# Kernel optimization log

Hardware: AMD Instinct MI355X
Metric: run time of the kernel (lower is better)

Reference implementation:

```python
import jax, jax.numpy as jnp
import numpy as np

DIM = 512
HEADS = 8
HEAD_DIM = DIM // HEADS

def setup_inputs() -> dict:
    key = jax.random.key(0)
    ks = jax.random.split(key, 5)
    s = 1.0 / np.sqrt(DIM)
    x = jax.random.normal(ks[0], (4, 2048, DIM), dtype=jnp.float32)
    w_qkv = jax.random.uniform(ks[1], (DIM, 3 * DIM), jnp.float32, -s, s)
    b_qkv = jax.random.uniform(ks[2], (3 * DIM,), jnp.float32, -s, s)
    w_out = jax.random.uniform(ks[3], (DIM, DIM), jnp.float32, -s, s)
    b_out = jax.random.uniform(ks[4], (DIM,), jnp.float32, -s, s)
    return {"x": x, "w_qkv": w_qkv, "b_qkv": b_qkv, "w_out": w_out, "b_out": b_out}

def reference(x, w_qkv, b_qkv, w_out, b_out):
    B, N, D = x.shape
    qkv = x @ w_qkv + b_qkv  # [B, N, 3D]
    qkv = qkv.reshape(B, N, 3, HEADS, HEAD_DIM).transpose(2, 0, 3, 1, 4)  # [3, B, H, N, hd]
    q, k, v = qkv[0], qkv[1], qkv[2]
    scale = 1.0 / np.sqrt(HEAD_DIM).astype(np.float32)
    attn = jnp.einsum('bhqd,bhkd->bhqk', q, k) * scale
    attn = jax.nn.softmax(attn, axis=-1)
    out = jnp.einsum('bhqk,bhkd->bhqd', attn, v)  # [B, H, N, hd]
    out = out.transpose(0, 2, 1, 3).reshape(B, N, D)
    return out @ w_out + b_out
```

## Files before the change

kernel.cpp:

```cpp
#include <hip/hip_runtime.h>

#define NB 4
#define NH 8
#define HD 64
#define DIMV 512
#define NSEQ 2048
#define QKVLD 1536
#define NTOK (NB*NSEQ)
#define KVB 64
#define QSCALE 0.18033688011112042f

typedef __attribute__((ext_vector_type(8))) short s8v;
typedef __attribute__((ext_vector_type(4))) float f4v;

typedef __attribute__((address_space(1))) void gvoid;
typedef __attribute__((address_space(3))) void lvoid;

__device__ __forceinline__ void load_lds16(const void* g, void* l){
  __builtin_amdgcn_global_load_lds((gvoid*)(void*)g, (lvoid*)l, 16, 0, 0);
}

__device__ __forceinline__ ushort f2bf(float f){
  unsigned u = __float_as_uint(f);
  u += 0x7fffu + ((u >> 16) & 1u);
  return (ushort)(u >> 16);
}

__device__ __forceinline__ unsigned pk2bf(float a, float b){
  return (unsigned)f2bf(a) | ((unsigned)f2bf(b) << 16);
}

__device__ __forceinline__ unsigned cvt_pk_bf16(float lo, float hi){
  unsigned r;
  asm("v_cvt_pk_bf16_f32 %0, %1, %2" : "=v"(r) : "v"(lo), "v"(hi));
  return r;
}
__device__ __forceinline__ float fexp2(float x){
  float r;
  asm("v_exp_f32 %0, %1" : "=v"(r) : "v"(x));
  return r;
}
__device__ __forceinline__ void plane32(unsigned &a, unsigned &b){
  asm("v_permlane32_swap_b32 %0, %1" : "+v"(a), "+v"(b));
}
__device__ __forceinline__ void plane16(unsigned &a, unsigned &b){
  asm("v_permlane16_swap_b32 %0, %1" : "+v"(a), "+v"(b));
}

__global__ __launch_bounds__(256) void k_prep(const float* __restrict__ x,
                                              ushort* __restrict__ xb,
                                              const float* __restrict__ w_qkv,
                                              ushort* __restrict__ wqkvT,
                                              const float* __restrict__ w_out,
                                              ushort* __restrict__ woutT){
  const int blk = blockIdx.x;
  const int tid = threadIdx.x;
  if (blk < 4096){
    const int i = blk * 256 + tid;
    float4 v = ((const float4*)x)[i];
    ushort4 o;
    o.x = f2bf(v.x); o.y = f2bf(v.y); o.z = f2bf(v.z); o.w = f2bf(v.w);
    ((ushort4*)xb)[i] = o;
    return;
  }
  __shared__ float t[32][33];
  const float* in; ushort* out; int C, bx, by;
  if (blk < 4864){
    const int idx = blk - 4096;
    in = w_qkv; out = wqkvT; C = QKVLD;
    bx = (idx % 48) * 32; by = (idx / 48) * 32;
  } else {
    const int idx = blk - 4864;
    in = w_out; out = woutT; C = DIMV;
    bx = (idx & 15) * 32; by = (idx >> 4) * 32;
  }
  const int tx = tid & 31, ty = tid >> 5;
  #pragma unroll
  for (int j = 0; j < 32; j += 8)
    t[ty + j][tx] = in[(size_t)(by + ty + j)*C + bx + tx];
  __syncthreads();
  #pragma unroll
  for (int j = 0; j < 32; j += 8)
    out[(size_t)(bx + ty + j)*DIMV + by + tx] = f2bf(t[tx][ty + j]);
}

template<int MODE, int NCT>
__global__ __launch_bounds__(256) void k_gemm(const ushort* __restrict__ A,
                                              const ushort* __restrict__ Bt,
                                              const float* __restrict__ bias,
                                              void* __restrict__ Cout,
                                              ushort* __restrict__ vtp,
                                              int N, int K){
  __shared__ ushort As[128*32];
  __shared__ ushort Bs[128*32];
  const int tid = threadIdx.x;
  const int w = tid >> 6, l = tid & 63;
  const int lr = l & 15, lg = l >> 4;
  const int wm = w >> 1, wn = w & 1;
  const int wg = blockIdx.x;
  const int xcd = wg & 7, idx = wg >> 3;
  const int tn = (idx % NCT) * 128;
  const int tm = (xcd * 8 + idx / NCT) * 128;
  const int srow = l >> 2;
  const int scol = (l & 3) * 8;
  f4v acc[4][4] = {};

  for (int kk = 0; kk < K; kk += 32){
    __syncthreads();
    #pragma unroll
    for (int c = 0; c < 2; ++c){
      const int r = (w*2 + c)*16 + srow;
      load_lds16(A  + (size_t)(tm + r)*K + kk + scol, (char*)As + (w*2 + c)*1024);
      load_lds16(Bt + (size_t)(tn + r)*K + kk + scol, (char*)Bs + (w*2 + c)*1024);
    }
    __syncthreads();
    s8v af[4], bf[4];
    #pragma unroll
    for (int i = 0; i < 4; ++i){
      af[i] = *(const s8v*)(&As[(wm*64 + i*16 + lr)*32 + lg*8]);
      bf[i] = *(const s8v*)(&Bs[(wn*64 + i*16 + lr)*32 + lg*8]);
    }
    #pragma unroll
    for (int mi = 0; mi < 4; ++mi)
      #pragma unroll
      for (int ni = 0; ni < 4; ++ni)
        acc[mi][ni] = __builtin_amdgcn_mfma_f32_16x16x32_bf16(af[mi], bf[ni], acc[mi][ni], 0, 0, 0);
  }

  if (MODE == 0){
    ushort* C = (ushort*)Cout;
    if (tn >= 2*DIMV){
      const int b = tm >> 11;
      const int n0 = (tm & (NSEQ-1)) + wm*64;
      #pragma unroll
      for (int ni = 0; ni < 4; ++ni){
        const int c = tn + wn*64 + ni*16 + lr;
        const int hd_i = c - 2*DIMV;
        const float bv = bias[c];
        ushort* vrow = vtp + ((size_t)(b*DIMV + hd_i))*NSEQ;
        #pragma unroll
        for (int mi = 0; mi < 4; ++mi){
          const int n = n0 + mi*16 + lg*4;
          uint2 pk;
          pk.x = pk2bf(acc[mi][ni][0] + bv, acc[mi][ni][1] + bv);
          pk.y = pk2bf(acc[mi][ni][2] + bv, acc[mi][ni][3] + bv);
          *(uint2*)(vrow + n) = pk;
        }
      }
    } else {
      #pragma unroll
      for (int ni = 0; ni < 4; ++ni){
        const int c = tn + wn*64 + ni*16 + lr;
        const float bv = bias[c];
        const float sc = (c < DIMV) ? QSCALE : 1.0f;
        #pragma unroll
        for (int mi = 0; mi < 4; ++mi)
          #pragma unroll
          for (int i = 0; i < 4; ++i){
            const int r = tm + wm*64 + mi*16 + lg*4 + i;
            C[(size_t)r*N + c] = f2bf((acc[mi][ni][i] + bv) * sc);
          }
      }
    }
  } else {
    float* C = (float*)Cout;
    #pragma unroll
    for (int ni = 0; ni < 4; ++ni){
      const int c = tn + wn*64 + ni*16 + lr;
      const float bv = bias[c];
      #pragma unroll
      for (int mi = 0; mi < 4; ++mi)
        #pragma unroll
        for (int i = 0; i < 4; ++i){
          const int r = tm + wm*64 + mi*16 + lg*4 + i;
          C[(size_t)r*N + c] = acc[mi][ni][i] + bv;
        }
    }
  }
}

__global__ __launch_bounds__(256, 4) void k_attn(const ushort* __restrict__ qkv,
                                                 const ushort* __restrict__ vt,
                                                 ushort* __restrict__ ao){
  __shared__ alignas(1024) char smem[2][16384];
  const int tid = threadIdx.x;
  const int w = tid >> 6, l = tid & 63;
  const int lr = l & 15, lg = l >> 4;
  const int wg = blockIdx.x;
  const int n = (wg & 7) * 128 + (wg >> 3);
  const int bh = n >> 5, xt = n & 31;
  const int b = bh >> 3, h = bh & 7;
  const int q0 = xt * 64 + w * 16;

  const ushort* qp = qkv + (size_t)(b*NSEQ + q0 + lr)*QKVLD + h*HD + lg*8;
  const s8v qf0 = *(const s8v*)(qp);
  const s8v qf1 = *(const s8v*)(qp + 32);

  const int r8 = l >> 3;
  const int lc = (l & 7) ^ r8;
  const int wbase = w * 16;
  const ushort* kg0 = qkv + (size_t)(b*NSEQ + wbase + r8)*QKVLD + DIMV + h*HD + lc*8;
  const ushort* kg1 = kg0 + (size_t)8*QKVLD;
  const ushort* vg0 = vt + (size_t)(bh*HD + wbase + r8)*NSEQ + lc*8;
  const ushort* vg1 = vg0 + (size_t)8*NSEQ;

  float lsum = 0.0f;
  f4v o[4] = {};

  load_lds16(kg0, &smem[0][ wbase   *128]);
  load_lds16(kg1, &smem[0][(wbase+8)*128]);
  load_lds16(vg0, &smem[0][ wbase   *128 + 8192]);
  load_lds16(vg1, &smem[0][(wbase+8)*128 + 8192]);
  kg0 += (size_t)KVB*QKVLD; kg1 += (size_t)KVB*QKVLD; vg0 += KVB; vg1 += KVB;

  const int swz = (lr & 7) << 4;
  const int ro0 = lr*128 + ((     lg*16) ^ swz);
  const int ro1 = lr*128 + ((64 + lg*16) ^ swz);

  #pragma unroll 2
  for (int kt = 0; kt < NSEQ/KVB; ++kt){
    const int cur = kt & 1;
    __syncthreads();

    if (kt + 1 < NSEQ/KVB){
      char* dst = &smem[cur^1][0];
      load_lds16(kg0, dst +  wbase   *128);
      load_lds16(kg1, dst + (wbase+8)*128);
      load_lds16(vg0, dst +  wbase   *128 + 8192);
      load_lds16(vg1, dst + (wbase+8)*128 + 8192);
      kg0 += (size_t)KVB*QKVLD; kg1 += (size_t)KVB*QKVLD; vg0 += KVB; vg1 += KVB;
    }

    const char* b0 = &smem[cur][0] + ro0;
    const char* b1 = &smem[cur][0] + ro1;

    f4v s0 = {0.f,0.f,0.f,0.f}, s1 = {0.f,0.f,0.f,0.f};
    f4v s2 = {0.f,0.f,0.f,0.f}, s3 = {0.f,0.f,0.f,0.f};
    __builtin_amdgcn_s_setprio(1);
    {
      const s8v a0 = *(const s8v*)(b0 +    0), a1 = *(const s8v*)(b1 +    0);
      const s8v a2 = *(const s8v*)(b0 + 2048), a3 = *(const s8v*)(b1 + 2048);
      s0 = __builtin_amdgcn_mfma_f32_16x16x32_bf16(a0, qf0, s0, 0,0,0);
      s0 = __builtin_amdgcn_mfma_f32_16x16x32_bf16(a1, qf1, s0, 0,0,0);
      s1 = __builtin_amdgcn_mfma_f32_16x16x32_bf16(a2, qf0, s1, 0,0,0);
      s1 = __builtin_amdgcn_mfma_f32_16x16x32_bf16(a3, qf1, s1, 0,0,0);
    }
    {
      const s8v a0 = *(const s8v*)(b0 + 4096), a1 = *(const s8v*)(b1 + 4096);
      const s8v a2 = *(const s8v*)(b0 + 6144), a3 = *(const s8v*)(b1 + 6144);
      s2 = __builtin_amdgcn_mfma_f32_16x16x32_bf16(a0, qf0, s2, 0,0,0);
      s2 = __builtin_amdgcn_mfma_f32_16x16x32_bf16(a1, qf1, s2, 0,0,0);
      s3 = __builtin_amdgcn_mfma_f32_16x16x32_bf16(a2, qf0, s3, 0,0,0);
      s3 = __builtin_amdgcn_mfma_f32_16x16x32_bf16(a3, qf1, s3, 0,0,0);
    }
    __builtin_amdgcn_s_setprio(0);

    union { uint4 u; s8v v; } pf0, pf1;
    {
      const float p0 = fexp2(s0[0]), p1 = fexp2(s0[1]);
      const float p2 = fexp2(s0[2]), p3 = fexp2(s0[3]);
      const float p4 = fexp2(s1[0]), p5 = fexp2(s1[1]);
      const float p6 = fexp2(s1[2]), p7 = fexp2(s1[3]);
      lsum += ((p0 + p1) + (p2 + p3)) + ((p4 + p5) + (p6 + p7));
      unsigned a = cvt_pk_bf16(p0, p1), bq = cvt_pk_bf16(p4, p5);
      plane32(a, bq); plane16(a, bq);
      unsigned c = cvt_pk_bf16(p2, p3), d = cvt_pk_bf16(p6, p7);
      plane32(c, d);  plane16(c, d);
      pf0.u.x = a; pf0.u.y = c; pf0.u.z = bq; pf0.u.w = d;
    }

    __builtin_amdgcn_s_setprio(1);
    {
      const s8v v0 = *(const s8v*)(b0 + 8192);
      const s8v v1 = *(const s8v*)(b0 + 10240);
      const s8v v2 = *(const s8v*)(b0 + 12288);
      const s8v v3 = *(const s8v*)(b0 + 14336);
      o[0] = __builtin_amdgcn_mfma_f32_16x16x32_bf16(v0, pf0.v, o[0], 0,0,0);
      o[1] = __builtin_amdgcn_mfma_f32_16x16x32_bf16(v1, pf0.v, o[1], 0,0,0);
      o[2] = __builtin_amdgcn_mfma_f32_16x16x32_bf16(v2, pf0.v, o[2], 0,0,0);
      o[3] = __builtin_amdgcn_mfma_f32_16x16x32_bf16(v3, pf0.v, o[3], 0,0,0);
    }
    __builtin_amdgcn_s_setprio(0);

    {
      const float p0 = fexp2(s2[0]), p1 = fexp2(s2[1]);
      const float p2 = fexp2(s2[2]), p3 = fexp2(s2[3]);
      const float p4 = fexp2(s3[0]), p5 = fexp2(s3[1]);
      const float p6 = fexp2(s3[2]), p7 = fexp2(s3[3]);
      lsum += ((p0 + p1) + (p2 + p3)) + ((p4 + p5) + (p6 + p7));
      unsigned a = cvt_pk_bf16(p0, p1), bq = cvt_pk_bf16(p4, p5);
      plane32(a, bq); plane16(a, bq);
      unsigned c = cvt_pk_bf16(p2, p3), d = cvt_pk_bf16(p6, p7);
      plane32(c, d);  plane16(c, d);
      pf1.u.x = a; pf1.u.y = c; pf1.u.z = bq; pf1.u.w = d;
    }

    __builtin_amdgcn_s_setprio(1);
    {
      const s8v v0 = *(const s8v*)(b1 + 8192);
      const s8v v1 = *(const s8v*)(b1 + 10240);
      const s8v v2 = *(const s8v*)(b1 + 12288);
      const s8v v3 = *(const s8v*)(b1 + 14336);
      o[0] = __builtin_amdgcn_mfma_f32_16x16x32_bf16(v0, pf1.v, o[0], 0,0,0);
      o[1] = __builtin_amdgcn_mfma_f32_16x16x32_bf16(v1, pf1.v, o[1], 0,0,0);
      o[2] = __builtin_amdgcn_mfma_f32_16x16x32_bf16(v2, pf1.v, o[2], 0,0,0);
      o[3] = __builtin_amdgcn_mfma_f32_16x16x32_bf16(v3, pf1.v, o[3], 0,0,0);
    }
    __builtin_amdgcn_s_setprio(0);
  }

  float lt = lsum;
  lt += __shfl_xor(lt, 16, 64);
  lt += __shfl_xor(lt, 32, 64);
  const float inv = 1.0f / lt;
  ushort* op = ao + (size_t)(b*NSEQ + q0 + lr)*DIMV + h*HD;
  #pragma unroll
  for (int ni = 0; ni < 4; ++ni){
    uint2 pk;
    pk.x = cvt_pk_bf16(o[ni][0]*inv, o[ni][1]*inv);
    pk.y = cvt_pk_bf16(o[ni][2]*inv, o[ni][3]*inv);
    *(uint2*)(op + ni*16 + lg*4) = pk;
  }
}


extern "C" void kernel_launch(void* const* d_in, const int* in_sizes, int n_in,
                              void* d_out, int out_size, void* d_ws, size_t ws_size,
                              hipStream_t stream) {
  (void)in_sizes; (void)n_in; (void)out_size; (void)ws_size;
  const float* x     = (const float*)d_in[0];
  const float* w_qkv = (const float*)d_in[1];
  const float* b_qkv = (const float*)d_in[2];
  const float* w_out = (const float*)d_in[3];
  const float* b_out = (const float*)d_in[4];
  float* out = (float*)d_out;

  char* ws = (char*)d_ws;
  ushort* xb    = (ushort*)(ws);
  ushort* wqkvT = (ushort*)(ws + 8388608);
  ushort* woutT = (ushort*)(ws + 8388608 + 1572864);
  ushort* qkv   = (ushort*)(ws + 10485760);
  ushort* vt    = (ushort*)(ws + 35651584);
  ushort* ao    = (ushort*)(ws + 44040192);

  k_prep<<<dim3(4096 + 768 + 256), 256, 0, stream>>>(x, xb, w_qkv, wqkvT, w_out, woutT);
  k_gemm<0,12><<<dim3(768), 256, 0, stream>>>(xb, wqkvT, b_qkv, qkv, vt, QKVLD, DIMV);
  k_attn<<<dim3(32*NB*NH), 256, 0, stream>>>(qkv, vt, ao);
  k_gemm<1,4><<<dim3(256), 256, 0, stream>>>(ao, woutT, b_out, out, nullptr, DIMV, DIMV);
}
```

Baseline: 103.3 us.

## Load V tiles directly from global into registers instead of staging in LDS

The attention kernel now fetches the transposed V fragments straight from global memory into registers each iteration, and shared memory is halved to hold only K tiles. This removes LDS staging and LDS reads for V and may raise occupancy, since each of the four waves reads the same V. In exchange, every wave issues redundant global loads for V, and their latency sits inside the loop with no prefetch ahead of the PV MMAs. The PV MMAs are also reordered to run together after both softmax blocks.

```diff
diff --git a/kernel.cpp b/kernel.cpp
--- a/kernel.cpp
+++ b/kernel.cpp
@@ -182,7 +182,7 @@
 __global__ __launch_bounds__(256, 4) void k_attn(const ushort* __restrict__ qkv,
                                                  const ushort* __restrict__ vt,
                                                  ushort* __restrict__ ao){
-  __shared__ alignas(1024) char smem[2][16384];
+  __shared__ alignas(1024) char smem[2][8192];
   const int tid = threadIdx.x;
   const int w = tid >> 6, l = tid & 63;
   const int lr = l & 15, lg = l >> 4;
@@ -201,17 +201,18 @@
   const int wbase = w * 16;
   const ushort* kg0 = qkv + (size_t)(b*NSEQ + wbase + r8)*QKVLD + DIMV + h*HD + lc*8;
   const ushort* kg1 = kg0 + (size_t)8*QKVLD;
-  const ushort* vg0 = vt + (size_t)(bh*HD + wbase + r8)*NSEQ + lc*8;
-  const ushort* vg1 = vg0 + (size_t)8*NSEQ;
+
+  const ushort* vp0 = vt + (size_t)(bh*HD +  0 + lr)*NSEQ + lg*8;
+  const ushort* vp1 = vt + (size_t)(bh*HD + 16 + lr)*NSEQ + lg*8;
+  const ushort* vp2 = vt + (size_t)(bh*HD + 32 + lr)*NSEQ + lg*8;
+  const ushort* vp3 = vt + (size_t)(bh*HD + 48 + lr)*NSEQ + lg*8;
 
   float lsum = 0.0f;
   f4v o[4] = {};
 
   load_lds16(kg0, &smem[0][ wbase   *128]);
   load_lds16(kg1, &smem[0][(wbase+8)*128]);
-  load_lds16(vg0, &smem[0][ wbase   *128 + 8192]);
-  load_lds16(vg1, &smem[0][(wbase+8)*128 + 8192]);
-  kg0 += (size_t)KVB*QKVLD; kg1 += (size_t)KVB*QKVLD; vg0 += KVB; vg1 += KVB;
+  kg0 += (size_t)KVB*QKVLD; kg1 += (size_t)KVB*QKVLD;
 
   const int swz = (lr & 7) << 4;
   const int ro0 = lr*128 + ((     lg*16) ^ swz);
@@ -222,13 +223,17 @@
     const int cur = kt & 1;
     __syncthreads();
 
+    const s8v vv00 = *(const s8v*)(vp0), vv01 = *(const s8v*)(vp0 + 32);
+    const s8v vv10 = *(const s8v*)(vp1), vv11 = *(const s8v*)(vp1 + 32);
+    const s8v vv20 = *(const s8v*)(vp2), vv21 = *(const s8v*)(vp2 + 32);
+    const s8v vv30 = *(const s8v*)(vp3), vv31 = *(const s8v*)(vp3 + 32);
+    vp0 += KVB; vp1 += KVB; vp2 += KVB; vp3 += KVB;
+
     if (kt + 1 < NSEQ/KVB){
       char* dst = &smem[cur^1][0];
       load_lds16(kg0, dst +  wbase   *128);
       load_lds16(kg1, dst + (wbase+8)*128);
-      load_lds16(vg0, dst +  wbase   *128 + 8192);
-      load_lds16(vg1, dst + (wbase+8)*128 + 8192);
-      kg0 += (size_t)KVB*QKVLD; kg1 += (size_t)KVB*QKVLD; vg0 += KVB; vg1 += KVB;
+      kg0 += (size_t)KVB*QKVLD; kg1 += (size_t)KVB*QKVLD;
     }
 
     const char* b0 = &smem[cur][0] + ro0;
@@ -268,20 +273,6 @@
       plane32(c, d);  plane16(c, d);
       pf0.u.x = a; pf0.u.y = c; pf0.u.z = bq; pf0.u.w = d;
     }
-
-    __builtin_amdgcn_s_setprio(1);
-    {
-      const s8v v0 = *(const s8v*)(b0 + 8192);
-      const s8v v1 = *(const s8v*)(b0 + 10240);
-      const s8v v2 = *(const s8v*)(b0 + 12288);
-      const s8v v3 = *(const s8v*)(b0 + 14336);
-      o[0] = __builtin_amdgcn_mfma_f32_16x16x32_bf16(v0, pf0.v, o[0], 0,0,0);
-      o[1] = __builtin_amdgcn_mfma_f32_16x16x32_bf16(v1, pf0.v, o[1], 0,0,0);
-      o[2] = __builtin_amdgcn_mfma_f32_16x16x32_bf16(v2, pf0.v, o[2], 0,0,0);
-      o[3] = __builtin_amdgcn_mfma_f32_16x16x32_bf16(v3, pf0.v, o[3], 0,0,0);
-    }
-    __builtin_amdgcn_s_setprio(0);
-
     {
       const float p0 = fexp2(s2[0]), p1 = fexp2(s2[1]);
       const float p2 = fexp2(s2[2]), p3 = fexp2(s2[3]);
@@ -296,16 +287,14 @@
     }
 
     __builtin_amdgcn_s_setprio(1);
-    {
-      const s8v v0 = *(const s8v*)(b1 + 8192);
-      const s8v v1 = *(const s8v*)(b1 + 10240);
-      const s8v v2 = *(const s8v*)(b1 + 12288);
-      const s8v v3 = *(const s8v*)(b1 + 14336);
-      o[0] = __builtin_amdgcn_mfma_f32_16x16x32_bf16(v0, pf1.v, o[0], 0,0,0);
-      o[1] = __builtin_amdgcn_mfma_f32_16x16x32_bf16(v1, pf1.v, o[1], 0,0,0);
-      o[2] = __builtin_amdgcn_mfma_f32_16x16x32_bf16(v2, pf1.v, o[2], 0,0,0);
-      o[3] = __builtin_amdgcn_mfma_f32_16x16x32_bf16(v3, pf1.v, o[3], 0,0,0);
-    }
+    o[0] = __builtin_amdgcn_mfma_f32_16x16x32_bf16(vv00, pf0.v, o[0], 0,0,0);
+    o[1] = __builtin_amdgcn_mfma_f32_16x16x32_bf16(vv10, pf0.v, o[1], 0,0,0);
+    o[2] = __builtin_amdgcn_mfma_f32_16x16x32_bf16(vv20, pf0.v, o[2], 0,0,0);
+    o[3] = __builtin_amdgcn_mfma_f32_16x16x32_bf16(vv30, pf0.v, o[3], 0,0,0);
+    o[0] = __builtin_amdgcn_mfma_f32_16x16x32_bf16(vv01, pf1.v, o[0], 0,0,0);
+    o[1] = __builtin_amdgcn_mfma_f32_16x16x32_bf16(vv11, pf1.v, o[1], 0,0,0);
+    o[2] = __builtin_amdgcn_mfma_f32_16x16x32_bf16(vv21, pf1.v, o[2], 0,0,0);
+    o[3] = __builtin_amdgcn_mfma_f32_16x16x32_bf16(vv31, pf1.v, o[3], 0,0,0);
     __builtin_amdgcn_s_setprio(0);
   }
 
```

Result: slower. 183.7 us (+77.9%).

## Process two 16-row query tiles per wave in attention to reuse K/V fragments

Applied to the files above, without the earlier changes.

Each wave in the attention kernel now handles 32 query rows (two 16-row MFMA tiles) instead of 16. Each block therefore covers 128 queries, and the grid halves to 512 blocks. Every K and V fragment read from LDS is reused by two MFMAs, which halves LDS traffic and K/V global loads per query. The cost is more registers (launch bounds lowered to 2 blocks per CU) and fewer blocks, which cuts occupancy and parallelism on a 256-CU device.

```diff
diff --git a/kernel.cpp b/kernel.cpp
--- a/kernel.cpp
+++ b/kernel.cpp
@@ -179,7 +179,7 @@
   }
 }
 
-__global__ __launch_bounds__(256, 4) void k_attn(const ushort* __restrict__ qkv,
+__global__ __launch_bounds__(256, 2) void k_attn(const ushort* __restrict__ qkv,
                                                  const ushort* __restrict__ vt,
                                                  ushort* __restrict__ ao){
   __shared__ alignas(1024) char smem[2][16384];
@@ -187,14 +187,17 @@
   const int w = tid >> 6, l = tid & 63;
   const int lr = l & 15, lg = l >> 4;
   const int wg = blockIdx.x;
-  const int n = (wg & 7) * 128 + (wg >> 3);
-  const int bh = n >> 5, xt = n & 31;
+  const int n = (wg & 7) * 64 + (wg >> 3);
+  const int bh = n >> 4, xt = n & 15;
   const int b = bh >> 3, h = bh & 7;
-  const int q0 = xt * 64 + w * 16;
-
-  const ushort* qp = qkv + (size_t)(b*NSEQ + q0 + lr)*QKVLD + h*HD + lg*8;
-  const s8v qf0 = *(const s8v*)(qp);
-  const s8v qf1 = *(const s8v*)(qp + 32);
+  const int q0 = xt * 128 + w * 32;
+
+  const ushort* qpA = qkv + (size_t)(b*NSEQ + q0 + lr)*QKVLD + h*HD + lg*8;
+  const ushort* qpB = qpA + (size_t)16*QKVLD;
+  const s8v qfA0 = *(const s8v*)(qpA);
+  const s8v qfA1 = *(const s8v*)(qpA + 32);
+  const s8v qfB0 = *(const s8v*)(qpB);
+  const s8v qfB1 = *(const s8v*)(qpB + 32);
 
   const int r8 = l >> 3;
   const int lc = (l & 7) ^ r8;
@@ -204,8 +207,8 @@
   const ushort* vg0 = vt + (size_t)(bh*HD + wbase + r8)*NSEQ + lc*8;
   const ushort* vg1 = vg0 + (size_t)8*NSEQ;
 
-  float lsum = 0.0f;
-  f4v o[4] = {};
+  float lsumA = 0.0f, lsumB = 0.0f;
+  f4v oA[4] = {}, oB[4] = {};
 
   load_lds16(kg0, &smem[0][ wbase   *128]);
   load_lds16(kg1, &smem[0][(wbase+8)*128]);
@@ -217,7 +220,6 @@
   const int ro0 = lr*128 + ((     lg*16) ^ swz);
   const int ro1 = lr*128 + ((64 + lg*16) ^ swz);
 
-  #pragma unroll 2
   for (int kt = 0; kt < NSEQ/KVB; ++kt){
     const int cur = kt & 1;
     __syncthreads();
@@ -234,92 +236,101 @@
     const char* b0 = &smem[cur][0] + ro0;
     const char* b1 = &smem[cur][0] + ro1;
 
-    f4v s0 = {0.f,0.f,0.f,0.f}, s1 = {0.f,0.f,0.f,0.f};
-    f4v s2 = {0.f,0.f,0.f,0.f}, s3 = {0.f,0.f,0.f,0.f};
+    f4v sA[4] = {}, sB[4] = {};
     __builtin_amdgcn_s_setprio(1);
+    #pragma unroll
+    for (int kb = 0; kb < 4; ++kb){
+      const s8v kf0 = *(const s8v*)(b0 + kb*2048);
+      const s8v kf1 = *(const s8v*)(b1 + kb*2048);
+      sA[kb] = __builtin_amdgcn_mfma_f32_16x16x32_bf16(kf0, qfA0, sA[kb], 0,0,0);
+      sA[kb] = __builtin_amdgcn_mfma_f32_16x16x32_bf16(kf1, qfA1, sA[kb], 0,0,0);
+      sB[kb] = __builtin_amdgcn_mfma_f32_16x16x32_bf16(kf0, qfB0, sB[kb], 0,0,0);
+      sB[kb] = __builtin_amdgcn_mfma_f32_16x16x32_bf16(kf1, qfB1, sB[kb], 0,0,0);
+    }
+    __builtin_amdgcn_s_setprio(0);
+
+    union { uint4 u; s8v v; } pfA0, pfA1, pfB0, pfB1;
     {
-      const s8v a0 = *(const s8v*)(b0 +    0), a1 = *(const s8v*)(b1 +    0);
-      const s8v a2 = *(const s8v*)(b0 + 2048), a3 = *(const s8v*)(b1 + 2048);
-      s0 = __builtin_amdgcn_mfma_f32_16x16x32_bf16(a0, qf0, s0, 0,0,0);
-      s0 = __builtin_amdgcn_mfma_f32_16x16x32_bf16(a1, qf1, s0, 0,0,0);
-      s1 = __builtin_amdgcn_mfma_f32_16x16x32_bf16(a2, qf0, s1, 0,0,0);
-      s1 = __builtin_amdgcn_mfma_f32_16x16x32_bf16(a3, qf1, s1, 0,0,0);
-    }
-    {
-      const s8v a0 = *(const s8v*)(b0 + 4096), a1 = *(const s8v*)(b1 + 4096);
-      const s8v a2 = *(const s8v*)(b0 + 6144), a3 = *(const s8v*)(b1 + 6144);
-      s2 = __builtin_amdgcn_mfma_f32_16x16x32_bf16(a0, qf0, s2, 0,0,0);
-      s2 = __builtin_amdgcn_mfma_f32_16x16x32_bf16(a1, qf1, s2, 0,0,0);
-      s3 = __builtin_amdgcn_mfma_f32_16x16x32_bf16(a2, qf0, s3, 0,0,0);
-      s3 = __builtin_amdgcn_mfma_f32_16x16x32_bf16(a3, qf1, s3, 0,0,0);
-    }
-    __builtin_amdgcn_s_setprio(0);
-
-    union { uint4 u; s8v v; } pf0, pf1;
-    {
-      const float p0 = fexp2(s0[0]), p1 = fexp2(s0[1]);
-      const float p2 = fexp2(s0[2]), p3 = fexp2(s0[3]);
-      const float p4 = fexp2(s1[0]), p5 = fexp2(s1[1]);
-      const float p6 = fexp2(s1[2]), p7 = fexp2(s1[3]);
-      lsum += ((p0 + p1) + (p2 + p3)) + ((p4 + p5) + (p6 + p7));
+      const float p0 = fexp2(sA[0][0]), p1 = fexp2(sA[0][1]);
+      const float p2 = fexp2(sA[0][2]), p3 = fexp2(sA[0][3]);
+      const float p4 = fexp2(sA[1][0]), p5 = fexp2(sA[1][1]);
+      const float p6 = fexp2(sA[1][2]), p7 = fexp2(sA[1][3]);
+      lsumA += ((p0 + p1) + (p2 + p3)) + ((p4 + p5) + (p6 + p7));
       unsigned a = cvt_pk_bf16(p0, p1), bq = cvt_pk_bf16(p4, p5);
       plane32(a, bq); plane16(a, bq);
       unsigned c = cvt_pk_bf16(p2, p3), d = cvt_pk_bf16(p6, p7);
       plane32(c, d);  plane16(c, d);
-      pf0.u.x = a; pf0.u.y = c; pf0.u.z = bq; pf0.u.w = d;
-    }
-
-    __builtin_amdgcn_s_setprio(1);
+      pfA0.u.x = a; pfA0.u.y = c; pfA0.u.z = bq; pfA0.u.w = d;
+    }
     {
-      const s8v v0 = *(const s8v*)(b0 + 8192);
-      const s8v v1 = *(const s8v*)(b0 + 10240);
-      const s8v v2 = *(const s8v*)(b0 + 12288);
-      const s8v v3 = *(const s8v*)(b0 + 14336);
-      o[0] = __builtin_amdgcn_mfma_f32_16x16x32_bf16(v0, pf0.v, o[0], 0,0,0);
-      o[1] = __builtin_amdgcn_mfma_f32_16x16x32_bf16(v1, pf0.v, o[1], 0,0,0);
-      o[2] = __builtin_amdgcn_mfma_f32_16x16x32_bf16(v2, pf0.v, o[2], 0,0,0);
-      o[3] = __builtin_amdgcn_mfma_f32_16x16x32_bf16(v3, pf0.v, o[3], 0,0,0);
-    }
-    __builtin_amdgcn_s_setprio(0);
-
-    {
-      const float p0 = fexp2(s2[0]), p1 = fexp2(s2[1]);
-      const float p2 = fexp2(s2[2]), p3 = fexp2(s2[3]);
-      const float p4 = fexp2(s3[0]), p5 = fexp2(s3[1]);
-      const float p6 = fexp2(s3[2]), p7 = fexp2(s3[3]);
-      lsum += ((p0 + p1) + (p2 + p3)) + ((p4 + p5) + (p6 + p7));
+      const float p0 = fexp2(sA[2][0]), p1 = fexp2(sA[2][1]);
+      const float p2 = fexp2(sA[2][2]), p3 = fexp2(sA[2][3]);
+      const float p4 = fexp2(sA[3][0]), p5 = fexp2(sA[3][1]);
+      const float p6 = fexp2(sA[3][2]), p7 = fexp2(sA[3][3]);
+      lsumA += ((p0 + p1) + (p2 + p3)) + ((p4 + p5) + (p6 + p7));
       unsigned a = cvt_pk_bf16(p0, p1), bq = cvt_pk_bf16(p4, p5);
       plane32(a, bq); plane16(a, bq);
       unsigned c = cvt_pk_bf16(p2, p3), d = cvt_pk_bf16(p6, p7);
       plane32(c, d);  plane16(c, d);
-      pf1.u.x = a; pf1.u.y = c; pf1.u.z = bq; pf1.u.w = d;
+      pfA1.u.x = a; pfA1.u.y = c; pfA1.u.z = bq; pfA1.u.w = d;
+    }
+    {
+      const float p0 = fexp2(sB[0][0]), p1 = fexp2(sB[0][1]);
+      const float p2 = fexp2(sB[0][2]), p3 = fexp2(sB[0][3]);
+      const float p4 = fexp2(sB[1][0]), p5 = fexp2(sB[1][1]);
+      const float p6 = fexp2(sB[1][2]), p7 = fexp2(sB[1][3]);
+      lsumB += ((p0 + p1) + (p2 + p3)) + ((p4 + p5) + (p6 + p7));
+      unsigned a = cvt_pk_bf16(p0, p1), bq = cvt_pk_bf16(p4, p5);
+      plane32(a, bq); plane16(a, bq);
+      unsigned c = cvt_pk_bf16(p2, p3), d = cvt_pk_bf16(p6, p7);
+      plane32(c, d);  plane16(c, d);
+      pfB0.u.x = a; pfB0.u.y = c; pfB0.u.z = bq; pfB0.u.w = d;
+    }
+    {
+      const float p0 = fexp2(sB[2][0]), p1 = fexp2(sB[2][1]);
+      const float p2 = fexp2(sB[2][2]), p3 = fexp2(sB[2][3]);
+      const float p4 = fexp2(sB[3][0]), p5 = fexp2(sB[3][1]);
+      const float p6 = fexp2(sB[3][2]), p7 = fexp2(sB[3][3]);
+      lsumB += ((p0 + p1) + (p2 + p3)) + ((p4 + p5) + (p6 + p7));
+      unsigned a = cvt_pk_bf16(p0, p1), bq = cvt_pk_bf16(p4, p5);
+      plane32(a, bq); plane16(a, bq);
+      unsigned c = cvt_pk_bf16(p2, p3), d = cvt_pk_bf16(p6, p7);
+      plane32(c, d);  plane16(c, d);
+      pfB1.u.x = a; pfB1.u.y = c; pfB1.u.z = bq; pfB1.u.w = d;
     }
 
     __builtin_amdgcn_s_setprio(1);
-    {
-      const s8v v0 = *(const s8v*)(b1 + 8192);
-      const s8v v1 = *(const s8v*)(b1 + 10240);
-      const s8v v2 = *(const s8v*)(b1 + 12288);
-      const s8v v3 = *(const s8v*)(b1 + 14336);
-      o[0] = __builtin_amdgcn_mfma_f32_16x16x32_bf16(v0, pf1.v, o[0], 0,0,0);
-      o[1] = __builtin_amdgcn_mfma_f32_16x16x32_bf16(v1, pf1.v, o[1], 0,0,0);
-      o[2] = __builtin_amdgcn_mfma_f32_16x16x32_bf16(v2, pf1.v, o[2], 0,0,0);
-      o[3] = __builtin_amdgcn_mfma_f32_16x16x32_bf16(v3, pf1.v, o[3], 0,0,0);
+    #pragma unroll
+    for (int ni = 0; ni < 4; ++ni){
+      const s8v vf0 = *(const s8v*)(b0 + 8192 + ni*2048);
+      const s8v vf1 = *(const s8v*)(b1 + 8192 + ni*2048);
+      oA[ni] = __builtin_amdgcn_mfma_f32_16x16x32_bf16(vf0, pfA0.v, oA[ni], 0,0,0);
+      oA[ni] = __builtin_amdgcn_mfma_f32_16x16x32_bf16(vf1, pfA1.v, oA[ni], 0,0,0);
+      oB[ni] = __builtin_amdgcn_mfma_f32_16x16x32_bf16(vf0, pfB0.v, oB[ni], 0,0,0);
+      oB[ni] = __builtin_amdgcn_mfma_f32_16x16x32_bf16(vf1, pfB1.v, oB[ni], 0,0,0);
     }
     __builtin_amdgcn_s_setprio(0);
   }
 
-  float lt = lsum;
-  lt += __shfl_xor(lt, 16, 64);
-  lt += __shfl_xor(lt, 32, 64);
-  const float inv = 1.0f / lt;
-  ushort* op = ao + (size_t)(b*NSEQ + q0 + lr)*DIMV + h*HD;
+  float ltA = lsumA;
+  ltA += __shfl_xor(ltA, 16, 64);
+  ltA += __shfl_xor(ltA, 32, 64);
+  float ltB = lsumB;
+  ltB += __shfl_xor(ltB, 16, 64);
+  ltB += __shfl_xor(ltB, 32, 64);
+  const float invA = 1.0f / ltA;
+  const float invB = 1.0f / ltB;
+  ushort* opA = ao + (size_t)(b*NSEQ + q0 + lr)*DIMV + h*HD;
+  ushort* opB = opA + (size_t)16*DIMV;
   #pragma unroll
   for (int ni = 0; ni < 4; ++ni){
     uint2 pk;
-    pk.x = cvt_pk_bf16(o[ni][0]*inv, o[ni][1]*inv);
-    pk.y = cvt_pk_bf16(o[ni][2]*inv, o[ni][3]*inv);
-    *(uint2*)(op + ni*16 + lg*4) = pk;
+    pk.x = cvt_pk_bf16(oA[ni][0]*invA, oA[ni][1]*invA);
+    pk.y = cvt_pk_bf16(oA[ni][2]*invA, oA[ni][3]*invA);
+    *(uint2*)(opA + ni*16 + lg*4) = pk;
+    pk.x = cvt_pk_bf16(oB[ni][0]*invB, oB[ni][1]*invB);
+    pk.y = cvt_pk_bf16(oB[ni][2]*invB, oB[ni][3]*invB);
+    *(uint2*)(opB + ni*16 + lg*4) = pk;
   }
 }
 
@@ -345,6 +356,6 @@
 
   k_prep<<<dim3(4096 + 768 + 256), 256, 0, stream>>>(x, xb, w_qkv, wqkvT, w_out, woutT);
   k_gemm<0,12><<<dim3(768), 256, 0, stream>>>(xb, wqkvT, b_qkv, qkv, vt, QKVLD, DIMV);
-  k_attn<<<dim3(32*NB*NH), 256, 0, stream>>>(qkv, vt, ao);
+  k_attn<<<dim3(512), 256, 0, stream>>>(qkv, vt, ao);
   k_gemm<1,4><<<dim3(256), 256, 0, stream>>>(ao, woutT, b_out, out, nullptr, DIMV, DIMV);
 }
```

Result: faster. 95.17 us (-7.8%).
